# Kernel optimization log

Hardware: AMD Instinct MI355X
Metric: run time of the kernel (lower is better)

The kernel has to match this reference:

```python
import jax, jax.numpy as jnp
import numpy as np

N = 1536       # number of agents in the group
T = 20         # track length (only last step used)
H = 64         # hidden_size
E = 16         # embadding_size
M = 128        # PNMLP_hidden_size


def setup_inputs() -> dict:
    key = jax.random.key(0)
    ks = jax.random.split(key, 8)
    s = lambda fan_in: 1.0 / np.sqrt(fan_in)
    return {
        "hidden_state": jax.random.normal(ks[0], (N, H), dtype=jnp.float32),
        "group_track": jax.random.normal(ks[1], (N, T, 2), dtype=jnp.float32),
        "We": jax.random.uniform(ks[2], (2, E), jnp.float32, -s(2), s(2)),
        "be": jax.random.uniform(ks[3], (E,), jnp.float32, -s(2), s(2)),
        "W1": jax.random.uniform(ks[4], (E + H, M), jnp.float32, -s(E + H), s(E + H)),
        "b1": jax.random.uniform(ks[5], (M,), jnp.float32, -s(E + H), s(E + H)),
        "W2": jax.random.uniform(ks[6], (M, H), jnp.float32, -s(M), s(M)),
        "b2": jax.random.uniform(ks[7], (H,), jnp.float32, -s(M), s(M)),
    }


def reference(hidden_state, group_track, We, be, W1, b1, W2, b2):
    # end positions of every track: [N, 2]
    end = group_track[:, -1, :]
    # rel[i, j] = end[j] - end[i]  (neighbor j relative to center i): [N, N, 2]
    rel = end[None, :, :] - end[:, None, :]
    # linear embedding of relative end positions: [N, N, E]
    emb = rel @ We + be
    # concat hidden state (same for all centers) with embedding: [N, N, E+H]
    h = jnp.broadcast_to(hidden_state[None, :, :], (rel.shape[0], rel.shape[1], hidden_state.shape[1]))
    x = jnp.concatenate((h, emb), axis=-1)
    # MLP [E+H -> M -> H] with ReLU after each linear (batch_norm=False)
    x = jax.nn.relu(x @ W1 + b1)
    x = jax.nn.relu(x @ W2 + b2)
    # max-pool over neighbors j for each center i: [N, H]
    return jnp.max(x, axis=1)
```

## Files before the change

### kernel.cpp

```cpp
#include <hip/hip_runtime.h>
#include <hip/hip_fp16.h>


#define NN 1536
#define HH 64
#define EE 16
#define MM 128
#define TT 20
#define NI 2
#define JSPLIT 8
#define NIGRP (NN / NI)
#define NTILE (96 / JSPLIT)

typedef _Float16 half8 __attribute__((ext_vector_type(8)));
typedef _Float16 half2v __attribute__((ext_vector_type(2)));
typedef float f32x4 __attribute__((ext_vector_type(4)));

union H8 { half8 v; half2v h2[4]; };

__global__ __launch_bounds__(128) void precompute_kernel(
    const float* __restrict__ hidden, const float* __restrict__ gt,
    const float* __restrict__ We, const float* __restrict__ be,
    const float* __restrict__ W1, const float* __restrict__ b1,
    const float* __restrict__ W2,
    _Float16* __restrict__ Q, _Float16* __restrict__ P,
    _Float16* __restrict__ W2T, float* __restrict__ out)
{
  const int j = blockIdx.x;
  const int m = threadIdx.x;
  const float* hrow = hidden + j * HH;
  float a = 0.f;
  #pragma unroll 8
  for (int h = 0; h < HH; ++h) a = fmaf(hrow[h], W1[h * MM + m], a);
  float ve0 = 0.f, ve1 = 0.f, cm = b1[m];
  #pragma unroll
  for (int e = 0; e < EE; ++e) {
    float w1e = W1[(HH + e) * MM + m];
    ve0 = fmaf(We[e], w1e, ve0);
    ve1 = fmaf(We[EE + e], w1e, ve1);
    cm  = fmaf(be[e], w1e, cm);
  }
  const float e0 = gt[j * (2 * TT) + 2 * (TT - 1)];
  const float e1 = gt[j * (2 * TT) + 2 * (TT - 1) + 1];
  const float p = fmaf(e0, ve0, e1 * ve1);
  P[j * MM + m] = (_Float16)p;
  Q[j * MM + m] = (_Float16)(a + p + cm);
  if (j < HH) W2T[j * MM + m] = (_Float16)W2[m * HH + j];
  if (m < HH) out[j * HH + m] = 0.f;
}

__global__ __launch_bounds__(64, 3) void pairmlp_max_kernel(
    const _Float16* __restrict__ Q, const _Float16* __restrict__ P,
    const _Float16* __restrict__ W2T, const float* __restrict__ b2,
    float* __restrict__ out)
{
  const int lane = threadIdx.x;
  const int quad = lane >> 4;
  const int lcol = lane & 15;
  const int ig = blockIdx.x % NIGRP;
  const int js = blockIdx.x / NIGRP;
  const int i0 = ig * NI;

  half8 bfrag[4][4];
  #pragma unroll
  for (int ct = 0; ct < 4; ++ct) {
    const _Float16* wrow = W2T + (ct * 16 + lcol) * MM + quad * 8;
    #pragma unroll
    for (int ks = 0; ks < 4; ++ks)
      bfrag[ct][ks] = *(const half8*)(wrow + ks * 32);
  }

  H8 pv[NI][4];
  #pragma unroll
  for (int ii = 0; ii < NI; ++ii) {
    const _Float16* prow = P + (i0 + ii) * MM + quad * 8;
    #pragma unroll
    for (int ks = 0; ks < 4; ++ks)
      pv[ii][ks].v = *(const half8*)(prow + ks * 32);
  }

  float rmax[NI][4];
  #pragma unroll
  for (int ii = 0; ii < NI; ++ii)
    #pragma unroll
    for (int ct = 0; ct < 4; ++ct) rmax[ii][ct] = -1e30f;

  const int jt0 = js * NTILE;
  const _Float16* qptr = Q + (jt0 * 16 + lcol) * MM + quad * 8;

  const half2v hz2 = {(_Float16)0.f, (_Float16)0.f};
  const f32x4 zc = {0.f, 0.f, 0.f, 0.f};

  #pragma unroll 1
  for (int t = 0; t < NTILE; ++t) {
    H8 q[4];
    #pragma unroll
    for (int ks = 0; ks < 4; ++ks)
      q[ks].v = *(const half8*)(qptr + ks * 32);
    qptr += 16 * MM;

    f32x4 acc[NI][4];
    #pragma unroll
    for (int ks = 0; ks < 4; ++ks) {
      #pragma unroll
      for (int ii = 0; ii < NI; ++ii) {
        H8 s;
        #pragma unroll
        for (int r = 0; r < 4; ++r) {
          half2v d = q[ks].h2[r] - pv[ii][ks].h2[r];
          s.h2[r] = __builtin_elementwise_max(d, hz2);
        }
        if (ks == 0) {
          #pragma unroll
          for (int ct = 0; ct < 4; ++ct)
            acc[ii][ct] = __builtin_amdgcn_mfma_f32_16x16x32_f16(s.v, bfrag[ct][0], zc, 0, 0, 0);
        } else {
          #pragma unroll
          for (int ct = 0; ct < 4; ++ct)
            acc[ii][ct] = __builtin_amdgcn_mfma_f32_16x16x32_f16(s.v, bfrag[ct][ks], acc[ii][ct], 0, 0, 0);
        }
      }
    }

    #pragma unroll
    for (int ii = 0; ii < NI; ++ii)
      #pragma unroll
      for (int ct = 0; ct < 4; ++ct) {
        const float m01 = fmaxf(acc[ii][ct][0], acc[ii][ct][1]);
        const float m23 = fmaxf(acc[ii][ct][2], acc[ii][ct][3]);
        rmax[ii][ct] = fmaxf(rmax[ii][ct], fmaxf(m01, m23));
      }
  }

  #pragma unroll
  for (int ii = 0; ii < NI; ++ii)
    #pragma unroll
    for (int ct = 0; ct < 4; ++ct) {
      float v = rmax[ii][ct];
      v = fmaxf(v, __shfl_xor(v, 16, 64));
      v = fmaxf(v, __shfl_xor(v, 32, 64));
      v = fmaxf(v + b2[ct * 16 + lcol], 0.f);
      if (quad == 0)
        atomicMax((unsigned*)(out + (i0 + ii) * HH + ct * 16 + lcol), __float_as_uint(v));
    }
}

extern "C" void kernel_launch(void* const* d_in, const int* in_sizes, int n_in,
                              void* d_out, int out_size, void* d_ws, size_t ws_size,
                              hipStream_t stream) {
  const float* hidden = (const float*)d_in[0];
  const float* gt     = (const float*)d_in[1];
  const float* We     = (const float*)d_in[2];
  const float* be     = (const float*)d_in[3];
  const float* W1     = (const float*)d_in[4];
  const float* b1     = (const float*)d_in[5];
  const float* W2     = (const float*)d_in[6];
  const float* b2     = (const float*)d_in[7];
  float* out = (float*)d_out;

  _Float16* Qh  = (_Float16*)d_ws;
  _Float16* Ph  = Qh + NN * MM;
  _Float16* W2T = Ph + NN * MM;

  precompute_kernel<<<NN, 128, 0, stream>>>(hidden, gt, We, be, W1, b1, W2, Qh, Ph, W2T, out);
  pairmlp_max_kernel<<<NIGRP * JSPLIT, 64, 0, stream>>>(Qh, Ph, W2T, b2, out);
}
```

Baseline: 126.3 us.

## Use four-wave blocks with one center row per wave in pair MLP kernel

Each block now has four waves and each wave handles a single center i, where before one wave handled two centers. The Q tile loads are now repeated per wave instead of shared across two centers inside one wave, though the four waves in a block read the same Q rows, which may hit in cache. Per-wave register use drops, which could raise occupancy, but less independent MFMA work per wave gives less latency hiding.

```diff
diff --git a/kernel.cpp b/kernel.cpp
--- a/kernel.cpp
+++ b/kernel.cpp
@@ -7,9 +7,8 @@
 #define EE 16
 #define MM 128
 #define TT 20
-#define NI 2
 #define JSPLIT 8
-#define NIGRP (NN / NI)
+#define NIGRP (NN / 4)
 #define NTILE (96 / JSPLIT)
 
 typedef _Float16 half8 __attribute__((ext_vector_type(8)));
@@ -49,17 +48,18 @@
   if (m < HH) out[j * HH + m] = 0.f;
 }
 
-__global__ __launch_bounds__(64, 3) void pairmlp_max_kernel(
+__global__ __launch_bounds__(256, 3) void pairmlp_max_kernel(
     const _Float16* __restrict__ Q, const _Float16* __restrict__ P,
     const _Float16* __restrict__ W2T, const float* __restrict__ b2,
     float* __restrict__ out)
 {
-  const int lane = threadIdx.x;
+  const int wave = threadIdx.x >> 6;
+  const int lane = threadIdx.x & 63;
   const int quad = lane >> 4;
   const int lcol = lane & 15;
   const int ig = blockIdx.x % NIGRP;
   const int js = blockIdx.x / NIGRP;
-  const int i0 = ig * NI;
+  const int i  = ig * 4 + wave;
 
   half8 bfrag[4][4];
   #pragma unroll
@@ -70,23 +70,17 @@
       bfrag[ct][ks] = *(const half8*)(wrow + ks * 32);
   }
 
-  H8 pv[NI][4];
-  #pragma unroll
-  for (int ii = 0; ii < NI; ++ii) {
-    const _Float16* prow = P + (i0 + ii) * MM + quad * 8;
+  H8 pv[4];
+  {
+    const _Float16* prow = P + i * MM + quad * 8;
     #pragma unroll
     for (int ks = 0; ks < 4; ++ks)
-      pv[ii][ks].v = *(const half8*)(prow + ks * 32);
+      pv[ks].v = *(const half8*)(prow + ks * 32);
   }
 
-  float rmax[NI][4];
-  #pragma unroll
-  for (int ii = 0; ii < NI; ++ii)
-    #pragma unroll
-    for (int ct = 0; ct < 4; ++ct) rmax[ii][ct] = -1e30f;
+  float rmax[4] = {-1e30f, -1e30f, -1e30f, -1e30f};
 
-  const int jt0 = js * NTILE;
-  const _Float16* qptr = Q + (jt0 * 16 + lcol) * MM + quad * 8;
+  const _Float16* qptr = Q + (js * NTILE * 16 + lcol) * MM + quad * 8;
 
   const half2v hz2 = {(_Float16)0.f, (_Float16)0.f};
   const f32x4 zc = {0.f, 0.f, 0.f, 0.f};
@@ -99,50 +93,43 @@
       q[ks].v = *(const half8*)(qptr + ks * 32);
     qptr += 16 * MM;
 
-    f32x4 acc[NI][4];
+    f32x4 acc[4];
     #pragma unroll
     for (int ks = 0; ks < 4; ++ks) {
+      H8 s;
       #pragma unroll
-      for (int ii = 0; ii < NI; ++ii) {
-        H8 s;
+      for (int r = 0; r < 4; ++r) {
+        half2v d = q[ks].h2[r] - pv[ks].h2[r];
+        s.h2[r] = __builtin_elementwise_max(d, hz2);
+      }
+      if (ks == 0) {
         #pragma unroll
-        for (int r = 0; r < 4; ++r) {
-          half2v d = q[ks].h2[r] - pv[ii][ks].h2[r];
-          s.h2[r] = __builtin_elementwise_max(d, hz2);
-        }
-        if (ks == 0) {
-          #pragma unroll
-          for (int ct = 0; ct < 4; ++ct)
-            acc[ii][ct] = __builtin_amdgcn_mfma_f32_16x16x32_f16(s.v, bfrag[ct][0], zc, 0, 0, 0);
-        } else {
-          #pragma unroll
-          for (int ct = 0; ct < 4; ++ct)
-            acc[ii][ct] = __builtin_amdgcn_mfma_f32_16x16x32_f16(s.v, bfrag[ct][ks], acc[ii][ct], 0, 0, 0);
-        }
+        for (int ct = 0; ct < 4; ++ct)
+          acc[ct] = __builtin_amdgcn_mfma_f32_16x16x32_f16(s.v, bfrag[ct][0], zc, 0, 0, 0);
+      } else {
+        #pragma unroll
+        for (int ct = 0; ct < 4; ++ct)
+          acc[ct] = __builtin_amdgcn_mfma_f32_16x16x32_f16(s.v, bfrag[ct][ks], acc[ct], 0, 0, 0);
       }
     }
 
     #pragma unroll
-    for (int ii = 0; ii < NI; ++ii)
-      #pragma unroll
-      for (int ct = 0; ct < 4; ++ct) {
-        const float m01 = fmaxf(acc[ii][ct][0], acc[ii][ct][1]);
-        const float m23 = fmaxf(acc[ii][ct][2], acc[ii][ct][3]);
-        rmax[ii][ct] = fmaxf(rmax[ii][ct], fmaxf(m01, m23));
-      }
+    for (int ct = 0; ct < 4; ++ct) {
+      const float m01 = fmaxf(acc[ct][0], acc[ct][1]);
+      const float m23 = fmaxf(acc[ct][2], acc[ct][3]);
+      rmax[ct] = fmaxf(rmax[ct], fmaxf(m01, m23));
+    }
   }
 
   #pragma unroll
-  for (int ii = 0; ii < NI; ++ii)
-    #pragma unroll
-    for (int ct = 0; ct < 4; ++ct) {
-      float v = rmax[ii][ct];
-      v = fmaxf(v, __shfl_xor(v, 16, 64));
-      v = fmaxf(v, __shfl_xor(v, 32, 64));
-      v = fmaxf(v + b2[ct * 16 + lcol], 0.f);
-      if (quad == 0)
-        atomicMax((unsigned*)(out + (i0 + ii) * HH + ct * 16 + lcol), __float_as_uint(v));
-    }
+  for (int ct = 0; ct < 4; ++ct) {
+    float v = rmax[ct];
+    v = fmaxf(v, __shfl_xor(v, 16, 64));
+    v = fmaxf(v, __shfl_xor(v, 32, 64));
+    v = fmaxf(v + b2[ct * 16 + lcol], 0.f);
+    if (quad == 0)
+      atomicMax((unsigned*)(out + i * HH + ct * 16 + lcol), __float_as_uint(v));
+  }
 }
 
 extern "C" void kernel_launch(void* const* d_in, const int* in_sizes, int n_in,
@@ -163,5 +150,5 @@
   _Float16* W2T = Ph + NN * MM;
 
   precompute_kernel<<<NN, 128, 0, stream>>>(hidden, gt, We, be, W1, b1, W2, Qh, Ph, W2T, out);
-  pairmlp_max_kernel<<<NIGRP * JSPLIT, 64, 0, stream>>>(Qh, Ph, W2T, b2, out);
+  pairmlp_max_kernel<<<NIGRP * JSPLIT, 256, 0, stream>>>(Qh, Ph, W2T, b2, out);
 }
```

After: 162.4 us. +28.5%, slower.

## Share W2 and Q tiles across four waves via swizzled LDS with async prefetch

Applied to the files above, without the earlier changes.

The pair-MLP kernel moves from one-wave blocks to 256-thread blocks of four waves covering 8 centers. W2^T and each 16-row Q tile are staged once in shared memory with direct global-to-LDS loads and double buffering, so all four waves reuse them instead of each wave loading its own copy into registers. The precompute kernel writes Q and W2^T in an XOR-swizzled layout so the LDS fragment reads avoid bank conflicts. In exchange, every tile iteration now ends in a block barrier, W2 fragments are reloaded from LDS on each tile, and the block count drops by a factor of four.

```diff
diff --git a/kernel.cpp b/kernel.cpp
--- a/kernel.cpp
+++ b/kernel.cpp
@@ -8,23 +8,27 @@
 #define MM 128
 #define TT 20
 #define NI 2
+#define IB 8
 #define JSPLIT 8
-#define NIGRP (NN / NI)
+#define NIGRP (NN / IB)
 #define NTILE (96 / JSPLIT)
 
 typedef _Float16 half8 __attribute__((ext_vector_type(8)));
-typedef _Float16 half2v __attribute__((ext_vector_type(2)));
 typedef float f32x4 __attribute__((ext_vector_type(4)));
 
-union H8 { half8 v; half2v h2[4]; };
+__device__ __forceinline__ void async16(const void* g, void* l) {
+  __builtin_amdgcn_global_load_lds(
+      (const __attribute__((address_space(1))) unsigned int*)g,
+      (__attribute__((address_space(3))) unsigned int*)l, 16, 0, 0);
+}
 
 __global__ __launch_bounds__(128) void precompute_kernel(
     const float* __restrict__ hidden, const float* __restrict__ gt,
     const float* __restrict__ We, const float* __restrict__ be,
     const float* __restrict__ W1, const float* __restrict__ b1,
     const float* __restrict__ W2,
-    _Float16* __restrict__ Q, _Float16* __restrict__ P,
-    _Float16* __restrict__ W2T, float* __restrict__ out)
+    _Float16* __restrict__ Qs, _Float16* __restrict__ P,
+    _Float16* __restrict__ W2Ts, float* __restrict__ out)
 {
   const int j = blockIdx.x;
   const int m = threadIdx.x;
@@ -44,40 +48,48 @@
   const float e1 = gt[j * (2 * TT) + 2 * (TT - 1) + 1];
   const float p = fmaf(e0, ve0, e1 * ve1);
   P[j * MM + m] = (_Float16)p;
-  Q[j * MM + m] = (_Float16)(a + p + cm);
-  if (j < HH) W2T[j * MM + m] = (_Float16)W2[m * HH + j];
+  const int swz = ((((m >> 3) ^ (j & 15)) << 3) | (m & 7));
+  Qs[j * MM + swz] = (_Float16)(a + p + cm);
+  if (j < HH) W2Ts[j * MM + swz] = (_Float16)W2[m * HH + j];
   if (m < HH) out[j * HH + m] = 0.f;
 }
 
-__global__ __launch_bounds__(64, 3) void pairmlp_max_kernel(
-    const _Float16* __restrict__ Q, const _Float16* __restrict__ P,
-    const _Float16* __restrict__ W2T, const float* __restrict__ b2,
+__global__ __launch_bounds__(256) void pairmlp_max_kernel(
+    const _Float16* __restrict__ Qs, const _Float16* __restrict__ P,
+    const _Float16* __restrict__ W2Ts, const float* __restrict__ b2,
     float* __restrict__ out)
 {
-  const int lane = threadIdx.x;
+  __shared__ __align__(16) _Float16 sW[HH * MM];
+  __shared__ __align__(16) _Float16 sQ[2][16 * MM];
+
+  const int tid  = threadIdx.x;
+  const int wave = tid >> 6;
+  const int lane = tid & 63;
   const int quad = lane >> 4;
   const int lcol = lane & 15;
   const int ig = blockIdx.x % NIGRP;
   const int js = blockIdx.x / NIGRP;
-  const int i0 = ig * NI;
+  const int i0 = ig * IB + wave * NI;
+  const int jt0 = js * NTILE;
 
-  half8 bfrag[4][4];
   #pragma unroll
-  for (int ct = 0; ct < 4; ++ct) {
-    const _Float16* wrow = W2T + (ct * 16 + lcol) * MM + quad * 8;
-    #pragma unroll
-    for (int ks = 0; ks < 4; ++ks)
-      bfrag[ct][ks] = *(const half8*)(wrow + ks * 32);
-  }
+  for (int r = 0; r < 4; ++r)
+    async16((const char*)W2Ts + tid * 16 + r * 4096, (char*)sW + tid * 16 + r * 4096);
+  async16((const char*)Qs + (size_t)jt0 * 4096 + tid * 16, (char*)sQ[0] + tid * 16);
 
-  H8 pv[NI][4];
+  half8 pv[NI][4];
   #pragma unroll
   for (int ii = 0; ii < NI; ++ii) {
     const _Float16* prow = P + (i0 + ii) * MM + quad * 8;
     #pragma unroll
     for (int ks = 0; ks < 4; ++ks)
-      pv[ii][ks].v = *(const half8*)(prow + ks * 32);
+      pv[ii][ks] = *(const half8*)(prow + ks * 32);
   }
+
+  int soff[4];
+  #pragma unroll
+  for (int ks = 0; ks < 4; ++ks)
+    soff[ks] = lcol * MM + ((((ks * 4 + quad) ^ lcol) & 15) << 3);
 
   float rmax[NI][4];
   #pragma unroll
@@ -85,39 +97,39 @@
     #pragma unroll
     for (int ct = 0; ct < 4; ++ct) rmax[ii][ct] = -1e30f;
 
-  const int jt0 = js * NTILE;
-  const _Float16* qptr = Q + (jt0 * 16 + lcol) * MM + quad * 8;
-
-  const half2v hz2 = {(_Float16)0.f, (_Float16)0.f};
+  const half8 hz = 0;
   const f32x4 zc = {0.f, 0.f, 0.f, 0.f};
 
-  #pragma unroll 1
+  __syncthreads();
+
+  #pragma unroll 2
   for (int t = 0; t < NTILE; ++t) {
-    H8 q[4];
-    #pragma unroll
-    for (int ks = 0; ks < 4; ++ks)
-      q[ks].v = *(const half8*)(qptr + ks * 32);
-    qptr += 16 * MM;
+    const int jn = (t + 1 < NTILE) ? (jt0 + t + 1) : jt0;
+    async16((const char*)Qs + (size_t)jn * 4096 + tid * 16, (char*)sQ[(t + 1) & 1] + tid * 16);
 
+    const _Float16* qb = sQ[t & 1];
     f32x4 acc[NI][4];
     #pragma unroll
     for (int ks = 0; ks < 4; ++ks) {
+      const half8 qg  = *(const half8*)(qb + soff[ks]);
+      const half8 bf0 = *(const half8*)(sW + soff[ks]);
+      const half8 bf1 = *(const half8*)(sW + soff[ks] + 16 * MM);
+      const half8 bf2 = *(const half8*)(sW + soff[ks] + 32 * MM);
+      const half8 bf3 = *(const half8*)(sW + soff[ks] + 48 * MM);
       #pragma unroll
       for (int ii = 0; ii < NI; ++ii) {
-        H8 s;
-        #pragma unroll
-        for (int r = 0; r < 4; ++r) {
-          half2v d = q[ks].h2[r] - pv[ii][ks].h2[r];
-          s.h2[r] = __builtin_elementwise_max(d, hz2);
-        }
+        half8 s = qg - pv[ii][ks];
+        s = __builtin_elementwise_max(s, hz);
         if (ks == 0) {
-          #pragma unroll
-          for (int ct = 0; ct < 4; ++ct)
-            acc[ii][ct] = __builtin_amdgcn_mfma_f32_16x16x32_f16(s.v, bfrag[ct][0], zc, 0, 0, 0);
+          acc[ii][0] = __builtin_amdgcn_mfma_f32_16x16x32_f16(s, bf0, zc, 0, 0, 0);
+          acc[ii][1] = __builtin_amdgcn_mfma_f32_16x16x32_f16(s, bf1, zc, 0, 0, 0);
+          acc[ii][2] = __builtin_amdgcn_mfma_f32_16x16x32_f16(s, bf2, zc, 0, 0, 0);
+          acc[ii][3] = __builtin_amdgcn_mfma_f32_16x16x32_f16(s, bf3, zc, 0, 0, 0);
         } else {
-          #pragma unroll
-          for (int ct = 0; ct < 4; ++ct)
-            acc[ii][ct] = __builtin_amdgcn_mfma_f32_16x16x32_f16(s.v, bfrag[ct][ks], acc[ii][ct], 0, 0, 0);
+          acc[ii][0] = __builtin_amdgcn_mfma_f32_16x16x32_f16(s, bf0, acc[ii][0], 0, 0, 0);
+          acc[ii][1] = __builtin_amdgcn_mfma_f32_16x16x32_f16(s, bf1, acc[ii][1], 0, 0, 0);
+          acc[ii][2] = __builtin_amdgcn_mfma_f32_16x16x32_f16(s, bf2, acc[ii][2], 0, 0, 0);
+          acc[ii][3] = __builtin_amdgcn_mfma_f32_16x16x32_f16(s, bf3, acc[ii][3], 0, 0, 0);
         }
       }
     }
@@ -130,6 +142,8 @@
         const float m23 = fmaxf(acc[ii][ct][2], acc[ii][ct][3]);
         rmax[ii][ct] = fmaxf(rmax[ii][ct], fmaxf(m01, m23));
       }
+
+    __syncthreads();
   }
 
   #pragma unroll
@@ -158,10 +172,10 @@
   const float* b2     = (const float*)d_in[7];
   float* out = (float*)d_out;
 
-  _Float16* Qh  = (_Float16*)d_ws;
-  _Float16* Ph  = Qh + NN * MM;
-  _Float16* W2T = Ph + NN * MM;
+  _Float16* Qs   = (_Float16*)d_ws;
+  _Float16* Ph   = Qs + NN * MM;
+  _Float16* W2Ts = Ph + NN * MM;
 
-  precompute_kernel<<<NN, 128, 0, stream>>>(hidden, gt, We, be, W1, b1, W2, Qh, Ph, W2T, out);
-  pairmlp_max_kernel<<<NIGRP * JSPLIT, 64, 0, stream>>>(Qh, Ph, W2T, b2, out);
+  precompute_kernel<<<NN, 128, 0, stream>>>(hidden, gt, We, be, W1, b1, W2, Qs, Ph, W2Ts, out);
+  pairmlp_max_kernel<<<NIGRP * JSPLIT, 256, 0, stream>>>(Qs, Ph, W2Ts, b2, out);
 }
```

After: 114.4 us. 9.4% less time.
